# Kernel optimization log

Measured on AMD Instinct MI355X. Metric: run time of the kernel, lower is better.

The kernel has to match this reference:

```python
import jax, jax.numpy as jnp
import numpy as np

B, H, NSTEPS = 4096, 1024, 10
T0, T1 = 0.0, 1.0


def setup_inputs() -> dict:
    key = jax.random.key(0)
    k0, k1, k2, k3 = jax.random.split(key, 4)
    s = 0.03  # keep tanh in active region
    return {
        "h0": jax.random.normal(k0, (B, H), dtype=jnp.float32),
        "W1": jax.random.normal(k1, (H + 1, 2 * H), dtype=jnp.float32) * s,
        "b1": jnp.zeros((2 * H,), dtype=jnp.float32),
        "W2": jax.random.normal(k2, (2 * H, 2 * H), dtype=jnp.float32) * s,
        "b2": jnp.zeros((2 * H,), dtype=jnp.float32),
        "W3": jax.random.normal(k3, (2 * H, H), dtype=jnp.float32) * s,
        "b3": jnp.zeros((H,), dtype=jnp.float32),
    }


def _ode_func(t, h, W1, b1, W2, b2, W3, b3):
    # time-dependent: append a column of t to the state  -> (B, H+1)
    tcol = jnp.full((h.shape[0], 1), t, dtype=h.dtype)
    x = jnp.concatenate([h, tcol], axis=1)
    x = jnp.tanh(x @ W1 + b1)
    x = jnp.tanh(x @ W2 + b2)
    return x @ W3 + b3  # (B, H)


def _integrate(h0, W1, b1, W2, b2, W3, b3):
    t = jnp.linspace(T0, T1, NSTEPS + 1, dtype=jnp.float32)
    dt = t[1:] - t[:-1]

    def f(ti, h):
        return _ode_func(ti, h, W1, b1, W2, b2, W3, b3)

    def step(h, td):
        ti, dti = td
        k1 = f(ti, h)
        k2 = f(ti + dti / 2, h + (dti / 2) * k1)
        k3 = f(ti + dti / 2, h + (dti / 2) * k2)
        k4 = f(ti + dti, h + dti * k3)
        h_next = h + (dti / 6) * (k1 + 2 * k2 + 2 * k3 + k4)
        return h_next, None

    h1, _ = jax.lax.scan(step, h0, (t[:-1], dt))
    return h1


def reference(h0, W1, b1, W2, b2, W3, b3):
    return _integrate(h0, W1, b1, W2, b2, W3, b3)
```

## Files before the change

kernel.cpp:

```cpp
#include <hip/hip_runtime.h>
#include <cstdint>
#include <cstddef>

typedef _Float16 half8 __attribute__((ext_vector_type(8)));
typedef float floatx4 __attribute__((ext_vector_type(4)));

typedef __attribute__((address_space(3))) unsigned lds_u32;
typedef const __attribute__((address_space(1))) unsigned glb_u32;

#define BK 64

__device__ __forceinline__ void glds16(const void* g, void* l) {
    __builtin_amdgcn_global_load_lds((glb_u32*)g, (lds_u32*)l, 16, 0, 0);
}

__device__ __forceinline__ float fast_tanh(float x) {
    float ax = fabsf(x);
    float e  = __expf(-2.0f * ax);
    float t  = (1.0f - e) / (1.0f + e);
    return x < 0.0f ? -t : t;
}

template <int MT, int NT, int NPX>
__device__ __forceinline__ void map_block(int id, int& mt, int& nt) {
    constexpr int NG  = NT / NPX;
    constexpr int XPG = 8 / NG;
    const int xcd  = id & 7;
    const int slot = id >> 3;
    nt = (xcd % NG) * NPX + (slot % NPX);
    mt = (xcd / NG) * (MT / XPG) + slot / NPX;
}

template <int TBM, int TBN, int MF, int NF, int NW>
__device__ __forceinline__ void gemm_acc_db(const _Float16* __restrict__ A,
                                            const _Float16* __restrict__ BT,
                                            size_t m0, size_t n0,
                                            int K, floatx4 acc[MF][NF]) {
    constexpr int CW = TBN / (16 * NF);
    constexpr int RW = TBM / (16 * MF);
    static_assert(RW * CW == NW, "wave grid must use all waves");
    constexpr int AH = TBM * 32;
    constexpr int BH = TBN * 32;

    __shared__ __align__(16) _Float16 As[2][TBM * BK];
    __shared__ __align__(16) _Float16 Bs[2][TBN * BK];

    const int tid  = threadIdx.x;
    const int lane = tid & 63;
    const int wid  = tid >> 6;

    const int srow = lane >> 2;
    const int skq  = (lane & 3) ^ ((lane >> 3) & 3);
    const int quad = lane >> 4;
    const int l16  = lane & 15;
    const int wm   = (wid / CW) * (16 * MF);
    const int wn   = (wid % CW) * (16 * NF);

#pragma unroll
    for (int i = 0; i < MF; ++i)
#pragma unroll
        for (int j = 0; j < NF; ++j)
            acc[i][j] = 0.0f;

    auto stage = [&](int buf, int k0) {
#pragma unroll
        for (int h = 0; h < 2; ++h) {
#pragma unroll
            for (int c = wid; c < TBM / 16; c += NW)
                glds16(A + (m0 + c * 16 + srow) * (size_t)K + k0 + h * 32 + skq * 8,
                       &As[buf][h * AH + c * 512]);
#pragma unroll
            for (int c = wid; c < TBN / 16; c += NW)
                glds16(BT + (n0 + c * 16 + srow) * (size_t)K + k0 + h * 32 + skq * 8,
                       &Bs[buf][h * BH + c * 512]);
        }
    };

    const int rdoff = l16 * 32 + ((quad ^ ((l16 >> 1) & 3)) << 3);

    stage(0, 0);
    int cur = 0;
    for (int k0 = 0; k0 < K; k0 += BK) {
        __syncthreads();
        if (k0 + BK < K) stage(cur ^ 1, k0 + BK);

#pragma unroll
        for (int h = 0; h < 2; ++h) {
            half8 av[MF], bv[NF];
#pragma unroll
            for (int i = 0; i < MF; ++i)
                av[i] = *(const half8*)(&As[cur][h * AH + ((wm >> 4) + i) * 512 + rdoff]);
#pragma unroll
            for (int j = 0; j < NF; ++j)
                bv[j] = *(const half8*)(&Bs[cur][h * BH + ((wn >> 4) + j) * 512 + rdoff]);
#pragma unroll
            for (int i = 0; i < MF; ++i)
#pragma unroll
                for (int j = 0; j < NF; ++j)
                    acc[i][j] = __builtin_amdgcn_mfma_f32_16x16x32_f16(av[i], bv[j], acc[i][j], 0, 0, 0);
        }
        cur ^= 1;
    }
}


template <bool WITH_T, int MT, int NT>
__global__ __launch_bounds__(512)
void gemm_bias_tanh(const _Float16* __restrict__ A, const _Float16* __restrict__ BT,
                    _Float16* __restrict__ out, const float* __restrict__ bias,
                    const float* __restrict__ brow, float t, int N, int K) {
    int mt, nt;
    map_block<MT, NT, 4>(blockIdx.x, mt, nt);
    const size_t bm0 = (size_t)mt * 128;
    const size_t bn0 = (size_t)nt * 128;

    floatx4 acc[4][2];
    gemm_acc_db<128, 128, 4, 2, 8>(A, BT, bm0, bn0, K, acc);

    const int tid  = threadIdx.x;
    const int lane = tid & 63;
    const int wid  = tid >> 6;
    const int quad = lane >> 4;
    const int l16  = lane & 15;
    const size_t m0 = bm0 + (size_t)(wid / 4) * 64;
    const size_t n0 = bn0 + (size_t)(wid % 4) * 32;

#pragma unroll
    for (int j = 0; j < 2; ++j) {
        const size_t col = n0 + j * 16 + l16;
        float b = bias[col];
        if (WITH_T) b += t * brow[col];
#pragma unroll
        for (int i = 0; i < 4; ++i) {
            const size_t rbase = m0 + i * 16 + quad * 4;
#pragma unroll
            for (int r = 0; r < 4; ++r) {
                out[(rbase + r) * (size_t)N + col] = (_Float16)fast_tanh(acc[i][j][r] + b);
            }
        }
    }
}

__global__ __launch_bounds__(512)
void gemm_k_stage(const _Float16* __restrict__ A, const _Float16* __restrict__ BT,
                  const float* __restrict__ bias, float* __restrict__ hstate,
                  float* __restrict__ accb, _Float16* __restrict__ x,
                  int stage, float c, float dt6, int N, int K) {
    int mt, nt;
    map_block<64, 8, 2>(blockIdx.x, mt, nt);
    const size_t bm0 = (size_t)mt * 64;
    const size_t bn0 = (size_t)nt * 128;

    floatx4 acc[2][2];
    gemm_acc_db<64, 128, 2, 2, 8>(A, BT, bm0, bn0, K, acc);

    const int tid  = threadIdx.x;
    const int lane = tid & 63;
    const int wid  = tid >> 6;
    const int quad = lane >> 4;
    const int l16  = lane & 15;
    const size_t m0 = bm0 + (size_t)(wid / 4) * 32;
    const size_t n0 = bn0 + (size_t)(wid % 4) * 32;

#pragma unroll
    for (int j = 0; j < 2; ++j) {
        const size_t col = n0 + j * 16 + l16;
        const float b = bias[col];
#pragma unroll
        for (int i = 0; i < 2; ++i) {
            const size_t rbase = m0 + i * 16 + quad * 4;
#pragma unroll
            for (int r = 0; r < 4; ++r) {
                const size_t idx = (rbase + r) * (size_t)N + col;
                const float k = acc[i][j][r] + b;
                if (stage == 0) {
                    accb[idx] = k;
                    x[idx] = (_Float16)(hstate[idx] + c * k);
                } else if (stage < 3) {
                    accb[idx] += 2.0f * k;
                    x[idx] = (_Float16)(hstate[idx] + c * k);
                } else {
                    const float hn = hstate[idx] + dt6 * (accb[idx] + k);
                    hstate[idx] = hn;
                    x[idx] = (_Float16)hn;
                }
            }
        }
    }
}

__global__ __launch_bounds__(256)
void transposeW(const float* __restrict__ W, _Float16* __restrict__ WT,
                int K, int N) {
    __shared__ float tile[32][33];
    const int tx = threadIdx.x;
    const int ty = threadIdx.y;
    const int n0 = blockIdx.x * 32;
    const int k0 = blockIdx.y * 32;
#pragma unroll
    for (int r = ty; r < 32; r += 8)
        tile[r][tx] = W[(size_t)(k0 + r) * N + n0 + tx];
    __syncthreads();
#pragma unroll
    for (int r = ty; r < 32; r += 8)
        WT[(size_t)(n0 + r) * K + k0 + tx] = (_Float16)tile[tx][r];
}

__global__ void copy_row(const float* __restrict__ W1, float* __restrict__ w1row, int N) {
    const int n = blockIdx.x * 256 + threadIdx.x;
    if (n < N) w1row[n] = W1[(size_t)1024 * N + n];
}

__global__ void init_h(const float* __restrict__ h0, float* __restrict__ hstate,
                       _Float16* __restrict__ x, int n) {
    const int i = blockIdx.x * 256 + threadIdx.x;
    if (i < n) {
        const float v = h0[i];
        hstate[i] = v;
        x[i] = (_Float16)v;
    }
}

extern "C" void kernel_launch(void* const* d_in, const int* in_sizes, int n_in,
                              void* d_out, int out_size, void* d_ws, size_t ws_size,
                              hipStream_t stream) {
    const int B = 4096, H = 1024, H2 = 2048;

    const float* h0 = (const float*)d_in[0];
    const float* W1 = (const float*)d_in[1];
    const float* b1 = (const float*)d_in[2];
    const float* W2 = (const float*)d_in[3];
    const float* b2 = (const float*)d_in[4];
    const float* W3 = (const float*)d_in[5];
    const float* b3 = (const float*)d_in[6];

    float* hstate = (float*)d_out;

    char* ws = (char*)d_ws;
    _Float16* x    = (_Float16*)ws; ws += (size_t)B * H  * 2;
    _Float16* a1   = (_Float16*)ws; ws += (size_t)B * H2 * 2;
    _Float16* a2   = (_Float16*)ws; ws += (size_t)B * H2 * 2;
    float*    accb = (float*)ws;    ws += (size_t)B * H  * 4;
    _Float16* W1T  = (_Float16*)ws; ws += (size_t)H2 * H  * 2;
    _Float16* W2T  = (_Float16*)ws; ws += (size_t)H2 * H2 * 2;
    _Float16* W3T  = (_Float16*)ws; ws += (size_t)H  * H2 * 2;
    float*   w1row = (float*)ws;    ws += (size_t)H2 * 4;

    const dim3 tblk(32, 8);
    transposeW<<<dim3(H2 / 32, H  / 32), tblk, 0, stream>>>(W1, W1T, H,  H2);
    transposeW<<<dim3(H2 / 32, H2 / 32), tblk, 0, stream>>>(W2, W2T, H2, H2);
    transposeW<<<dim3(H  / 32, H2 / 32), tblk, 0, stream>>>(W3, W3T, H2, H);
    copy_row<<<dim3(H2 / 256), 256, 0, stream>>>(W1, w1row, H2);
    init_h<<<dim3((B * H + 255) / 256), 256, 0, stream>>>(h0, hstate, x, B * H);

    const float dt  = 0.1f;
    const float dt2 = 0.05f;
    const float dt6 = dt / 6.0f;

    const dim3 blk(512);
    const int g12 = (B / 128) * (H2 / 128);
    const int g3  = (B / 64) * (H / 128);

    for (int s = 0; s < 10; ++s) {
        const float ti = (float)s * dt;

        gemm_bias_tanh<true , 32, 16><<<g12, blk, 0, stream>>>(x,  W1T, a1, b1, w1row, ti,       H2, H);
        gemm_bias_tanh<false, 32, 16><<<g12, blk, 0, stream>>>(a1, W2T, a2, b2, nullptr, 0.f,    H2, H2);
        gemm_k_stage<<<g3, blk, 0, stream>>>(a2, W3T, b3, hstate, accb, x, 0, dt2, dt6, H, H2);

        gemm_bias_tanh<true , 32, 16><<<g12, blk, 0, stream>>>(x,  W1T, a1, b1, w1row, ti + dt2, H2, H);
        gemm_bias_tanh<false, 32, 16><<<g12, blk, 0, stream>>>(a1, W2T, a2, b2, nullptr, 0.f,    H2, H2);
        gemm_k_stage<<<g3, blk, 0, stream>>>(a2, W3T, b3, hstate, accb, x, 1, dt2, dt6, H, H2);

        gemm_bias_tanh<true , 32, 16><<<g12, blk, 0, stream>>>(x,  W1T, a1, b1, w1row, ti + dt2, H2, H);
        gemm_bias_tanh<false, 32, 16><<<g12, blk, 0, stream>>>(a1, W2T, a2, b2, nullptr, 0.f,    H2, H2);
        gemm_k_stage<<<g3, blk, 0, stream>>>(a2, W3T, b3, hstate, accb, x, 2, dt,  dt6, H, H2);

        gemm_bias_tanh<true , 32, 16><<<g12, blk, 0, stream>>>(x,  W1T, a1, b1, w1row, ti + dt,  H2, H);
        gemm_bias_tanh<false, 32, 16><<<g12, blk, 0, stream>>>(a1, W2T, a2, b2, nullptr, 0.f,    H2, H2);
        gemm_k_stage<<<g3, blk, 0, stream>>>(a2, W3T, b3, hstate, accb, x, 3, dt,  dt6, H, H2);
    }
}
```

Measured before the change: 4.295 ms.

## Replace double-buffered GEMM with 4-stage LDS pipeline and larger tiles

Replaces the two-buffer BK=64 main loop with a four-slot ring of 32-wide K slices. Each slice is prefetched three phases ahead, and the code waits with explicit vmcnt counts and raw barriers instead of __syncthreads. MFMA issue is raised with setprio. Block tiles grow: the tanh GEMMs go to 256x128 with 4x4 fragments per wave, and the k-stage GEMM goes to 128x128 with 256 threads, which raises per-wave reuse. The cost is more registers per wave and fewer blocks in the grid, which may hurt occupancy or load balance.

```diff
diff --git a/kernel.cpp b/kernel.cpp
--- a/kernel.cpp
+++ b/kernel.cpp
@@ -8,11 +8,16 @@
 typedef __attribute__((address_space(3))) unsigned lds_u32;
 typedef const __attribute__((address_space(1))) unsigned glb_u32;
 
-#define BK 64
-
 __device__ __forceinline__ void glds16(const void* g, void* l) {
     __builtin_amdgcn_global_load_lds((glb_u32*)g, (lds_u32*)l, 16, 0, 0);
 }
+
+template <int N>
+__device__ __forceinline__ void waitv() {
+    asm volatile("s_waitcnt vmcnt(%0)" :: "n"(N) : "memory");
+}
+
+template <int N> struct IC { static constexpr int value = N; };
 
 __device__ __forceinline__ float fast_tanh(float x) {
     float ax = fabsf(x);
@@ -32,18 +37,20 @@
 }
 
 template <int TBM, int TBN, int MF, int NF, int NW>
-__device__ __forceinline__ void gemm_acc_db(const _Float16* __restrict__ A,
-                                            const _Float16* __restrict__ BT,
-                                            size_t m0, size_t n0,
-                                            int K, floatx4 acc[MF][NF]) {
+__device__ __forceinline__ void gemm_acc_pipe(const _Float16* __restrict__ A,
+                                              const _Float16* __restrict__ BT,
+                                              size_t m0, size_t n0,
+                                              int K, floatx4 acc[MF][NF]) {
     constexpr int CW = TBN / (16 * NF);
     constexpr int RW = TBM / (16 * MF);
     static_assert(RW * CW == NW, "wave grid must use all waves");
-    constexpr int AH = TBM * 32;
-    constexpr int BH = TBN * 32;
-
-    __shared__ __align__(16) _Float16 As[2][TBM * BK];
-    __shared__ __align__(16) _Float16 Bs[2][TBN * BK];
+    constexpr int NCA = TBM / 16;
+    constexpr int NCB = TBN / 16;
+    static_assert(NCA % NW == 0 && NCB % NW == 0, "uniform per-wave staging");
+    constexpr int LPW = NCA / NW + NCB / NW;
+
+    __shared__ __align__(16) _Float16 As[4][TBM * 32];
+    __shared__ __align__(16) _Float16 Bs[4][TBN * 32];
 
     const int tid  = threadIdx.x;
     const int lane = tid & 63;
@@ -62,71 +69,79 @@
         for (int j = 0; j < NF; ++j)
             acc[i][j] = 0.0f;
 
-    auto stage = [&](int buf, int k0) {
-#pragma unroll
-        for (int h = 0; h < 2; ++h) {
-#pragma unroll
-            for (int c = wid; c < TBM / 16; c += NW)
-                glds16(A + (m0 + c * 16 + srow) * (size_t)K + k0 + h * 32 + skq * 8,
-                       &As[buf][h * AH + c * 512]);
-#pragma unroll
-            for (int c = wid; c < TBN / 16; c += NW)
-                glds16(BT + (n0 + c * 16 + srow) * (size_t)K + k0 + h * 32 + skq * 8,
-                       &Bs[buf][h * BH + c * 512]);
-        }
+    auto stage = [&](int p) {
+        const int buf = p & 3;
+        const int kk  = p * 32 + skq * 8;
+#pragma unroll
+        for (int c = wid; c < NCA; c += NW)
+            glds16(A + (m0 + c * 16 + srow) * (size_t)K + kk, &As[buf][c * 512]);
+#pragma unroll
+        for (int c = wid; c < NCB; c += NW)
+            glds16(BT + (n0 + c * 16 + srow) * (size_t)K + kk, &Bs[buf][c * 512]);
     };
 
     const int rdoff = l16 * 32 + ((quad ^ ((l16 >> 1) & 3)) << 3);
-
-    stage(0, 0);
-    int cur = 0;
-    for (int k0 = 0; k0 < K; k0 += BK) {
-        __syncthreads();
-        if (k0 + BK < K) stage(cur ^ 1, k0 + BK);
-
-#pragma unroll
-        for (int h = 0; h < 2; ++h) {
-            half8 av[MF], bv[NF];
-#pragma unroll
-            for (int i = 0; i < MF; ++i)
-                av[i] = *(const half8*)(&As[cur][h * AH + ((wm >> 4) + i) * 512 + rdoff]);
+    const int NP = K / 32;
+
+    stage(0); stage(1); stage(2);
+
+    auto phase = [&](int t, auto d) {
+        constexpr int D = decltype(d)::value;
+        if constexpr (D == 3) stage(t + 3);
+        waitv<D * LPW>();
+        __builtin_amdgcn_s_barrier();
+        asm volatile("" ::: "memory");
+        const _Float16* Ab = &As[t & 3][0];
+        const _Float16* Bb = &Bs[t & 3][0];
+        half8 av[MF], bv[NF];
+#pragma unroll
+        for (int i = 0; i < MF; ++i)
+            av[i] = *(const half8*)(Ab + ((wm >> 4) + i) * 512 + rdoff);
+#pragma unroll
+        for (int j = 0; j < NF; ++j)
+            bv[j] = *(const half8*)(Bb + ((wn >> 4) + j) * 512 + rdoff);
+        __builtin_amdgcn_s_setprio(1);
+#pragma unroll
+        for (int i = 0; i < MF; ++i)
 #pragma unroll
             for (int j = 0; j < NF; ++j)
-                bv[j] = *(const half8*)(&Bs[cur][h * BH + ((wn >> 4) + j) * 512 + rdoff]);
-#pragma unroll
-            for (int i = 0; i < MF; ++i)
-#pragma unroll
-                for (int j = 0; j < NF; ++j)
-                    acc[i][j] = __builtin_amdgcn_mfma_f32_16x16x32_f16(av[i], bv[j], acc[i][j], 0, 0, 0);
-        }
-        cur ^= 1;
-    }
+                acc[i][j] = __builtin_amdgcn_mfma_f32_16x16x32_f16(av[i], bv[j], acc[i][j], 0, 0, 0);
+        __builtin_amdgcn_s_setprio(0);
+        asm volatile("s_waitcnt lgkmcnt(0)" ::: "memory");
+        __builtin_amdgcn_s_barrier();
+        asm volatile("" ::: "memory");
+    };
+
+    for (int t = 0; t + 3 < NP; ++t) phase(t, IC<3>{});
+    phase(NP - 3, IC<2>{});
+    phase(NP - 2, IC<1>{});
+    phase(NP - 1, IC<0>{});
 }
 
 
 template <bool WITH_T, int MT, int NT>
-__global__ __launch_bounds__(512)
+__global__ __launch_bounds__(512, 2)
 void gemm_bias_tanh(const _Float16* __restrict__ A, const _Float16* __restrict__ BT,
                     _Float16* __restrict__ out, const float* __restrict__ bias,
                     const float* __restrict__ brow, float t, int N, int K) {
     int mt, nt;
     map_block<MT, NT, 4>(blockIdx.x, mt, nt);
-    const size_t bm0 = (size_t)mt * 128;
+    const size_t bm0 = (size_t)mt * 256;
     const size_t bn0 = (size_t)nt * 128;
 
-    floatx4 acc[4][2];
-    gemm_acc_db<128, 128, 4, 2, 8>(A, BT, bm0, bn0, K, acc);
+    floatx4 acc[4][4];
+    gemm_acc_pipe<256, 128, 4, 4, 8>(A, BT, bm0, bn0, K, acc);
 
     const int tid  = threadIdx.x;
     const int lane = tid & 63;
     const int wid  = tid >> 6;
     const int quad = lane >> 4;
     const int l16  = lane & 15;
-    const size_t m0 = bm0 + (size_t)(wid / 4) * 64;
-    const size_t n0 = bn0 + (size_t)(wid % 4) * 32;
-
-#pragma unroll
-    for (int j = 0; j < 2; ++j) {
+    const size_t m0 = bm0 + (size_t)(wid >> 1) * 64;
+    const size_t n0 = bn0 + (size_t)(wid & 1) * 64;
+
+#pragma unroll
+    for (int j = 0; j < 4; ++j) {
         const size_t col = n0 + j * 16 + l16;
         float b = bias[col];
         if (WITH_T) b += t * brow[col];
@@ -141,33 +156,33 @@
     }
 }
 
-__global__ __launch_bounds__(512)
+__global__ __launch_bounds__(256, 1)
 void gemm_k_stage(const _Float16* __restrict__ A, const _Float16* __restrict__ BT,
                   const float* __restrict__ bias, float* __restrict__ hstate,
                   float* __restrict__ accb, _Float16* __restrict__ x,
                   int stage, float c, float dt6, int N, int K) {
     int mt, nt;
-    map_block<64, 8, 2>(blockIdx.x, mt, nt);
-    const size_t bm0 = (size_t)mt * 64;
+    map_block<32, 8, 2>(blockIdx.x, mt, nt);
+    const size_t bm0 = (size_t)mt * 128;
     const size_t bn0 = (size_t)nt * 128;
 
-    floatx4 acc[2][2];
-    gemm_acc_db<64, 128, 2, 2, 8>(A, BT, bm0, bn0, K, acc);
+    floatx4 acc[4][4];
+    gemm_acc_pipe<128, 128, 4, 4, 4>(A, BT, bm0, bn0, K, acc);
 
     const int tid  = threadIdx.x;
     const int lane = tid & 63;
     const int wid  = tid >> 6;
     const int quad = lane >> 4;
     const int l16  = lane & 15;
-    const size_t m0 = bm0 + (size_t)(wid / 4) * 32;
-    const size_t n0 = bn0 + (size_t)(wid % 4) * 32;
-
-#pragma unroll
-    for (int j = 0; j < 2; ++j) {
+    const size_t m0 = bm0 + (size_t)(wid >> 1) * 64;
+    const size_t n0 = bn0 + (size_t)(wid & 1) * 64;
+
+#pragma unroll
+    for (int j = 0; j < 4; ++j) {
         const size_t col = n0 + j * 16 + l16;
         const float b = bias[col];
 #pragma unroll
-        for (int i = 0; i < 2; ++i) {
+        for (int i = 0; i < 4; ++i) {
             const size_t rbase = m0 + i * 16 + quad * 4;
 #pragma unroll
             for (int r = 0; r < 4; ++r) {
@@ -257,27 +272,28 @@
     const float dt2 = 0.05f;
     const float dt6 = dt / 6.0f;
 
-    const dim3 blk(512);
-    const int g12 = (B / 128) * (H2 / 128);
-    const int g3  = (B / 64) * (H / 128);
+    const dim3 blk12(512);
+    const dim3 blk3(256);
+    const int g12 = (B / 256) * (H2 / 128);
+    const int g3  = (B / 128) * (H / 128);
 
     for (int s = 0; s < 10; ++s) {
         const float ti = (float)s * dt;
 
-        gemm_bias_tanh<true , 32, 16><<<g12, blk, 0, stream>>>(x,  W1T, a1, b1, w1row, ti,       H2, H);
-        gemm_bias_tanh<false, 32, 16><<<g12, blk, 0, stream>>>(a1, W2T, a2, b2, nullptr, 0.f,    H2, H2);
-        gemm_k_stage<<<g3, blk, 0, stream>>>(a2, W3T, b3, hstate, accb, x, 0, dt2, dt6, H, H2);
-
-        gemm_bias_tanh<true , 32, 16><<<g12, blk, 0, stream>>>(x,  W1T, a1, b1, w1row, ti + dt2, H2, H);
-        gemm_bias_tanh<false, 32, 16><<<g12, blk, 0, stream>>>(a1, W2T, a2, b2, nullptr, 0.f,    H2, H2);
-        gemm_k_stage<<<g3, blk, 0, stream>>>(a2, W3T, b3, hstate, accb, x, 1, dt2, dt6, H, H2);
-
-        gemm_bias_tanh<true , 32, 16><<<g12, blk, 0, stream>>>(x,  W1T, a1, b1, w1row, ti + dt2, H2, H);
-        gemm_bias_tanh<false, 32, 16><<<g12, blk, 0, stream>>>(a1, W2T, a2, b2, nullptr, 0.f,    H2, H2);
-        gemm_k_stage<<<g3, blk, 0, stream>>>(a2, W3T, b3, hstate, accb, x, 2, dt,  dt6, H, H2);
-
-        gemm_bias_tanh<true , 32, 16><<<g12, blk, 0, stream>>>(x,  W1T, a1, b1, w1row, ti + dt,  H2, H);
-        gemm_bias_tanh<false, 32, 16><<<g12, blk, 0, stream>>>(a1, W2T, a2, b2, nullptr, 0.f,    H2, H2);
-        gemm_k_stage<<<g3, blk, 0, stream>>>(a2, W3T, b3, hstate, accb, x, 3, dt,  dt6, H, H2);
-    }
-}
+        gemm_bias_tanh<true , 16, 16><<<g12, blk12, 0, stream>>>(x,  W1T, a1, b1, w1row, ti,       H2, H);
+        gemm_bias_tanh<false, 16, 16><<<g12, blk12, 0, stream>>>(a1, W2T, a2, b2, nullptr, 0.f,    H2, H2);
+        gemm_k_stage<<<g3, blk3, 0, stream>>>(a2, W3T, b3, hstate, accb, x, 0, dt2, dt6, H, H2);
+
+        gemm_bias_tanh<true , 16, 16><<<g12, blk12, 0, stream>>>(x,  W1T, a1, b1, w1row, ti + dt2, H2, H);
+        gemm_bias_tanh<false, 16, 16><<<g12, blk12, 0, stream>>>(a1, W2T, a2, b2, nullptr, 0.f,    H2, H2);
+        gemm_k_stage<<<g3, blk3, 0, stream>>>(a2, W3T, b3, hstate, accb, x, 1, dt2, dt6, H, H2);
+
+        gemm_bias_tanh<true , 16, 16><<<g12, blk12, 0, stream>>>(x,  W1T, a1, b1, w1row, ti + dt2, H2, H);
+        gemm_bias_tanh<false, 16, 16><<<g12, blk12, 0, stream>>>(a1, W2T, a2, b2, nullptr, 0.f,    H2, H2);
+        gemm_k_stage<<<g3, blk3, 0, stream>>>(a2, W3T, b3, hstate, accb, x, 2, dt,  dt6, H, H2);
+
+        gemm_bias_tanh<true , 16, 16><<<g12, blk12, 0, stream>>>(x,  W1T, a1, b1, w1row, ti + dt,  H2, H);
+        gemm_bias_tanh<false, 16, 16><<<g12, blk12, 0, stream>>>(a1, W2T, a2, b2, nullptr, 0.f,    H2, H2);
+        gemm_k_stage<<<g3, blk3, 0, stream>>>(a2, W3T, b3, hstate, accb, x, 3, dt,  dt6, H, H2);
+    }
+}
```

Result: slower. 5.637 ms (+31.3%).

## Add 256x128-tile double-buffered GEMM kernel for the second layer

Applied to the files above, without the earlier changes.

Adds a dedicated kernel for the 2048x2048 middle layer that computes a 256x128 output tile per block, with each wave holding a 64x64 accumulator (4x4 MFMA tiles). It stages both A and B through double-buffered swizzled LDS with direct global-to-LDS loads and raises MFMA wave priority. Larger per-wave tiles raise arithmetic intensity and cut LDS reads per MFMA. The cost is more registers and LDS, and half as many blocks, which may hurt occupancy and load balance.

```diff
diff --git a/kernel.cpp b/kernel.cpp
--- a/kernel.cpp
+++ b/kernel.cpp
@@ -130,6 +130,104 @@
         const size_t col = n0 + j * 16 + l16;
         float b = bias[col];
         if (WITH_T) b += t * brow[col];
+#pragma unroll
+        for (int i = 0; i < 4; ++i) {
+            const size_t rbase = m0 + i * 16 + quad * 4;
+#pragma unroll
+            for (int r = 0; r < 4; ++r) {
+                out[(rbase + r) * (size_t)N + col] = (_Float16)fast_tanh(acc[i][j][r] + b);
+            }
+        }
+    }
+}
+
+__global__ __launch_bounds__(512, 2)
+void gemm_tanh2(const _Float16* __restrict__ A, const _Float16* __restrict__ BT,
+                _Float16* __restrict__ out, const float* __restrict__ bias,
+                int N, int K) {
+    int mt, nt;
+    map_block<16, 16, 4>(blockIdx.x, mt, nt);
+    const size_t bm0 = (size_t)mt * 256;
+    const size_t bn0 = (size_t)nt * 128;
+
+    constexpr int AH = 256 * 32;
+    constexpr int BH = 128 * 32;
+
+    __shared__ __align__(16) _Float16 As[2][256 * 64];
+    __shared__ __align__(16) _Float16 Bs[2][128 * 64];
+
+    const int tid  = threadIdx.x;
+    const int lane = tid & 63;
+    const int wid  = tid >> 6;
+    const int srow = lane >> 2;
+    const int skq  = (lane & 3) ^ ((lane >> 3) & 3);
+    const int quad = lane >> 4;
+    const int l16  = lane & 15;
+    const int wmc  = (wid >> 1) * 4;
+    const int wnc  = (wid & 1) * 4;
+    const int rdoff = l16 * 32 + ((quad ^ ((l16 >> 1) & 3)) << 3);
+
+    floatx4 acc[4][4];
+#pragma unroll
+    for (int i = 0; i < 4; ++i)
+#pragma unroll
+        for (int j = 0; j < 4; ++j)
+            acc[i][j] = 0.0f;
+
+    auto stage_all = [&](int b, int k0) {
+        const int kk = k0 + skq * 8;
+#pragma unroll
+        for (int u = 0; u < 4; ++u) {
+            const int c  = wid + u * 8;
+            const int ra = c >> 1, kh = c & 1;
+            glds16(A + (bm0 + ra * 16 + srow) * (size_t)K + kk + kh * 32,
+                   &As[b][kh * AH + ra * 512]);
+        }
+#pragma unroll
+        for (int u = 0; u < 2; ++u) {
+            const int c  = wid + u * 8;
+            const int rb = c >> 1, kh = c & 1;
+            glds16(BT + (bn0 + rb * 16 + srow) * (size_t)K + kk + kh * 32,
+                   &Bs[b][kh * BH + rb * 512]);
+        }
+    };
+
+    stage_all(0, 0);
+    const int NP = K / 64;
+    int cur = 0;
+    for (int t = 0; t < NP; ++t) {
+        __syncthreads();
+        if (t + 1 < NP) stage_all(cur ^ 1, (t + 1) * 64);
+
+        half8 bv[2][4];
+#pragma unroll
+        for (int h = 0; h < 2; ++h)
+#pragma unroll
+            for (int j = 0; j < 4; ++j)
+                bv[h][j] = *(const half8*)(&Bs[cur][h * BH + (wnc + j) * 512 + rdoff]);
+
+#pragma unroll
+        for (int i = 0; i < 4; ++i) {
+            half8 a0 = *(const half8*)(&As[cur][0 * AH + (wmc + i) * 512 + rdoff]);
+            half8 a1 = *(const half8*)(&As[cur][1 * AH + (wmc + i) * 512 + rdoff]);
+            __builtin_amdgcn_s_setprio(1);
+#pragma unroll
+            for (int j = 0; j < 4; ++j)
+                acc[i][j] = __builtin_amdgcn_mfma_f32_16x16x32_f16(a0, bv[0][j], acc[i][j], 0, 0, 0);
+#pragma unroll
+            for (int j = 0; j < 4; ++j)
+                acc[i][j] = __builtin_amdgcn_mfma_f32_16x16x32_f16(a1, bv[1][j], acc[i][j], 0, 0, 0);
+            __builtin_amdgcn_s_setprio(0);
+        }
+        cur ^= 1;
+    }
+
+    const size_t m0 = bm0 + (size_t)(wid >> 1) * 64;
+    const size_t n0 = bn0 + (size_t)(wid & 1) * 64;
+#pragma unroll
+    for (int j = 0; j < 4; ++j) {
+        const size_t col = n0 + j * 16 + l16;
+        const float b = bias[col];
 #pragma unroll
         for (int i = 0; i < 4; ++i) {
             const size_t rbase = m0 + i * 16 + quad * 4;
@@ -229,8 +327,8 @@
     const float* h0 = (const float*)d_in[0];
     const float* W1 = (const float*)d_in[1];
     const float* b1 = (const float*)d_in[2];
+    const float* b2 = (const float*)d_in[4];
     const float* W2 = (const float*)d_in[3];
-    const float* b2 = (const float*)d_in[4];
     const float* W3 = (const float*)d_in[5];
     const float* b3 = (const float*)d_in[6];
 
@@ -258,26 +356,27 @@
     const float dt6 = dt / 6.0f;
 
     const dim3 blk(512);
-    const int g12 = (B / 128) * (H2 / 128);
-    const int g3  = (B / 64) * (H / 128);
+    const int g1 = (B / 128) * (H2 / 128);
+    const int g2 = (B / 256) * (H2 / 128);
+    const int g3 = (B / 64) * (H / 128);
 
     for (int s = 0; s < 10; ++s) {
         const float ti = (float)s * dt;
 
-        gemm_bias_tanh<true , 32, 16><<<g12, blk, 0, stream>>>(x,  W1T, a1, b1, w1row, ti,       H2, H);
-        gemm_bias_tanh<false, 32, 16><<<g12, blk, 0, stream>>>(a1, W2T, a2, b2, nullptr, 0.f,    H2, H2);
+        gemm_bias_tanh<true , 32, 16><<<g1, blk, 0, stream>>>(x,  W1T, a1, b1, w1row, ti,       H2, H);
+        gemm_tanh2<<<g2, blk, 0, stream>>>(a1, W2T, a2, b2, H2, H2);
         gemm_k_stage<<<g3, blk, 0, stream>>>(a2, W3T, b3, hstate, accb, x, 0, dt2, dt6, H, H2);
 
-        gemm_bias_tanh<true , 32, 16><<<g12, blk, 0, stream>>>(x,  W1T, a1, b1, w1row, ti + dt2, H2, H);
-        gemm_bias_tanh<false, 32, 16><<<g12, blk, 0, stream>>>(a1, W2T, a2, b2, nullptr, 0.f,    H2, H2);
+        gemm_bias_tanh<true , 32, 16><<<g1, blk, 0, stream>>>(x,  W1T, a1, b1, w1row, ti + dt2, H2, H);
+        gemm_tanh2<<<g2, blk, 0, stream>>>(a1, W2T, a2, b2, H2, H2);
         gemm_k_stage<<<g3, blk, 0, stream>>>(a2, W3T, b3, hstate, accb, x, 1, dt2, dt6, H, H2);
 
-        gemm_bias_tanh<true , 32, 16><<<g12, blk, 0, stream>>>(x,  W1T, a1, b1, w1row, ti + dt2, H2, H);
-        gemm_bias_tanh<false, 32, 16><<<g12, blk, 0, stream>>>(a1, W2T, a2, b2, nullptr, 0.f,    H2, H2);
+        gemm_bias_tanh<true , 32, 16><<<g1, blk, 0, stream>>>(x,  W1T, a1, b1, w1row, ti + dt2, H2, H);
+        gemm_tanh2<<<g2, blk, 0, stream>>>(a1, W2T, a2, b2, H2, H2);
         gemm_k_stage<<<g3, blk, 0, stream>>>(a2, W3T, b3, hstate, accb, x, 2, dt,  dt6, H, H2);
 
-        gemm_bias_tanh<true , 32, 16><<<g12, blk, 0, stream>>>(x,  W1T, a1, b1, w1row, ti + dt,  H2, H);
-        gemm_bias_tanh<false, 32, 16><<<g12, blk, 0, stream>>>(a1, W2T, a2, b2, nullptr, 0.f,    H2, H2);
+        gemm_bias_tanh<true , 32, 16><<<g1, blk, 0, stream>>>(x,  W1T, a1, b1, w1row, ti + dt,  H2, H);
+        gemm_tanh2<<<g2, blk, 0, stream>>>(a1, W2T, a2, b2, H2, H2);
         gemm_k_stage<<<g3, blk, 0, stream>>>(a2, W3T, b3, hstate, accb, x, 3, dt,  dt6, H, H2);
     }
 }
```

Measured after the change: 4.685 ms. +9.1%, slower.
